# Kernel optimization log

Measured on AMD Instinct MI355X. Metric: run time of the kernel, lower is better.

## Reference

```python
import jax, jax.numpy as jnp
import numpy as np
from jax import lax

N, CIN, COUT, T, V, S = 64, 64, 64, 256, 25, 3
REL = CIN // 8  # 8, per __init__ branch for in_channels=64


def setup_inputs() -> dict:
    key = jax.random.key(0)
    ks = jax.random.split(key, 22)
    rn = lambda i, shape, s=0.05: jax.random.normal(ks[i], shape, jnp.float32) * s
    return dict(
        x=jax.random.normal(ks[0], (N, CIN, T, V), jnp.float32),
        A=rn(1, (S, V, V), 0.2),                 # adaptive PA parameter
        alpha=jnp.asarray(0.1, jnp.float32),     # unit_gcn alpha (scalar)
        w1=rn(2, (S, REL, CIN)), b1=rn(3, (S, REL)),
        w2=rn(4, (S, REL, CIN)), b2=rn(5, (S, REL)),
        w3=rn(6, (S, COUT, CIN)), b3=rn(7, (S, COUT)),
        w4=rn(8, (S, COUT, REL)), b4=rn(9, (S, COUT)),
        pm_w1=rn(10, (S, REL, 2 * REL)), pm_b1=rn(11, (S, REL)),
        pm_w2=rn(12, (S, REL, REL)), pm_b2=rn(13, (S, REL)),
        dw_w=rn(14, (S, REL, 1, 3, 3)),          # depthwise 3x3, groups=REL
        proj_w=rn(15, (S, COUT, REL)),           # aux_proj, no bias
        beta=rn(16, (S,), 0.01), gamma=rn(17, (S,), 0.01),
        bn_w=jnp.ones((COUT,), jnp.float32), bn_b=jnp.zeros((COUT,), jnp.float32),
    )


def _sorgc(x, Ai, alpha, w1, b1, w2, b2, w3, b3, w4, b4,
           pw1, pb1, pw2, pb2, dww, pjw, beta, gamma):
    # x: (N, C, T, V)
    xm = x.mean(axis=2)                                            # (N,C,V) -- 1x1 conv is linear, so conv then mean == mean then conv
    x1 = jnp.einsum('ncv,rc->nrv', xm, w1) + b1[:, None]           # (N,R,V)
    x2 = jnp.einsum('ncv,rc->nrv', xm, w2) + b2[:, None]
    x3 = jnp.einsum('nctv,oc->notv', x, w3) + b3[:, None, None]    # (N,O,T,V)
    q1 = jnp.tanh(x1[:, :, :, None] - x2[:, :, None, :])           # (N,R,V,V)
    psi = jnp.broadcast_to(x2[:, :, :, None], q1.shape)
    phi = jnp.broadcast_to(x2[:, :, None, :], q1.shape)
    pair = jnp.concatenate([psi, phi], axis=1)                     # (N,2R,V,V)
    h = jax.nn.relu(jnp.einsum('npuv,rp->nruv', pair, pw1) + pb1[:, None, None])
    q2 = jnp.einsum('npuv,rp->nruv', h, pw2) + pb2[:, None, None]
    q_all = q1 + gamma * q2
    R = (jnp.einsum('nruv,or->nouv', q_all, w4) + b4[:, None, None]) * alpha + Ai[None, None]
    # aux branch: depthwise 3x3 conv -> avgpool3x3 (count_include_pad) -> tanh -> 1x1 proj
    Ra = lax.conv_general_dilated(q1, dww, (1, 1), [(1, 1), (1, 1)],
                                  dimension_numbers=('NCHW', 'OIHW', 'NCHW'),
                                  feature_group_count=q1.shape[1])
    Ra = lax.reduce_window(Ra, 0.0, lax.add, (1, 1, 3, 3), (1, 1, 1, 1),
                           [(0, 0), (0, 0), (1, 1), (1, 1)]) / 9.0
    Ra = jnp.tanh(Ra)
    Ra = jnp.einsum('nruv,or->nouv', Ra, pjw)                      # (N,O,V,V)
    R = R + beta * Ra
    return jnp.einsum('ncuv,nctv->nctu', R, x3)                    # (N,O,T,V)


def reference(x, A, alpha, w1, b1, w2, b2, w3, b3, w4, b4,
              pm_w1, pm_b1, pm_w2, pm_b2, dw_w, proj_w, beta, gamma, bn_w, bn_b):
    y = None
    for i in range(S):
        z = _sorgc(x, A[i], alpha, w1[i], b1[i], w2[i], b2[i], w3[i], b3[i],
                   w4[i], b4[i], pm_w1[i], pm_b1[i], pm_w2[i], pm_b2[i],
                   dw_w[i], proj_w[i], beta[i], gamma[i])
        y = z if y is None else y + z
    # BatchNorm2d (training-mode batch statistics), eps=1e-5
    mu = y.mean(axis=(0, 2, 3), keepdims=True)
    var = y.var(axis=(0, 2, 3), keepdims=True)
    y = (y - mu) * lax.rsqrt(var + 1e-5) * bn_w[None, :, None, None] + bn_b[None, :, None, None]
    y = y + x  # residual (in_channels == out_channels -> identity down)
    return jax.nn.relu(y)
```

## Files before the change

kernel.cpp:

```cpp
#include <hip/hip_runtime.h>


#define WS_R_BYTE   409600
#define WS_BN_BYTE  17711104

typedef __attribute__((ext_vector_type(8))) short bf16x8;
typedef __attribute__((ext_vector_type(4))) float f32x4;

static __device__ __forceinline__ unsigned short f2bf(float f) {
    unsigned int u = __float_as_uint(f);
    u += 0x7fff + ((u >> 16) & 1);
    return (unsigned short)(u >> 16);
}
static __device__ __forceinline__ float bf2f(unsigned short s) {
    return __uint_as_float(((unsigned int)s) << 16);
}

__global__ __launch_bounds__(256) void k_xm(const float* __restrict__ x,
                                            float* __restrict__ ws) {
    int idx = blockIdx.x * 256 + threadIdx.x;
    int n = idx / 1600;
    int cv = idx % 1600;
    int c = cv / 25, v = cv % 25;
    const float* xp = x + (n * 64 + c) * 6400 + v;
    float s = 0.f;
    #pragma unroll 8
    for (int t = 0; t < 256; t++) s += xp[t * 25];
    ws[idx] = s * (1.f / 256.f);
}

__global__ __launch_bounds__(512) void k_small(
    const float* __restrict__ ws, unsigned short* __restrict__ Rg,
    const float* __restrict__ A, const float* __restrict__ alphap,
    const float* __restrict__ w1, const float* __restrict__ b1,
    const float* __restrict__ w2, const float* __restrict__ b2,
    const float* __restrict__ w4, const float* __restrict__ b4,
    const float* __restrict__ pw1, const float* __restrict__ pb1,
    const float* __restrict__ pw2, const float* __restrict__ pb2,
    const float* __restrict__ dww, const float* __restrict__ pjw,
    const float* __restrict__ beta, const float* __restrict__ gamma) {
    __shared__ float sm[15000];
    const int tid = threadIdx.x;
    const int s = blockIdx.x >> 6;
    const int n = blockIdx.x & 63;
    const float alpha = alphap[0];
    const float gam = gamma[s], bet = beta[s];

    for (int i = tid; i < 1600; i += 512) sm[5000 + i] = ws[n * 1600 + i];
    __syncthreads();

    for (int i = tid; i < 400; i += 512) {
        int half = i / 200, j = i % 200;
        int r = j / 25, k = j % 25;
        const float* w = (half ? w2 : w1) + (s * 8 + r) * 64;
        float acc = (half ? b2 : b1)[s * 8 + r];
        for (int c = 0; c < 64; c++) acc += w[c] * sm[5000 + c * 25 + k];
        sm[6600 + i] = acc;
    }
    __syncthreads();

    for (int i = tid; i < 5400; i += 512) {
        if (i < 5000) {
            int r = i / 625, uv = i % 625, u = uv / 25, v = uv % 25;
            sm[i] = tanhf(sm[6600 + r * 25 + u] - sm[6800 + r * 25 + v]);
        } else {
            int i2 = i - 5000;
            int half = i2 / 200, j = i2 % 200;
            int r = j / 25, k = j % 25;
            float acc = 0.f;
            for (int p = 0; p < 8; p++)
                acc += pw1[(s * 8 + r) * 16 + half * 8 + p] * sm[6800 + p * 25 + k];
            sm[7000 + i2] = acc;
        }
    }
    __syncthreads();

    for (int i = tid; i < 5000; i += 512) {
        int r = i / 625, uv = i % 625, u = uv / 25, v = uv % 25;
        float t = sm[7000 + r * 25 + u] + sm[7200 + r * 25 + v] + pb1[s * 8 + r];
        sm[10000 + i] = t > 0.f ? t : 0.f;
    }
    __syncthreads();

    for (int i = tid; i < 5000; i += 512) {
        int r = i / 625, uv = i % 625;
        float q2 = pb2[s * 8 + r];
        for (int p = 0; p < 8; p++)
            q2 += pw2[(s * 8 + r) * 8 + p] * sm[10000 + p * 625 + uv];
        sm[5000 + i] = sm[i] + gam * q2;
    }
    __syncthreads();

    for (int i = tid; i < 5000; i += 512) {
        int r = i / 625, uv = i % 625, u = uv / 25, v = uv % 25;
        float acc = 0.f;
        for (int di = 0; di < 3; di++) {
            int uu = u + di - 1;
            if (uu < 0 || uu > 24) continue;
            for (int dj = 0; dj < 3; dj++) {
                int vv = v + dj - 1;
                if (vv < 0 || vv > 24) continue;
                acc += sm[r * 625 + uu * 25 + vv] * dww[(s * 8 + r) * 9 + di * 3 + dj];
            }
        }
        sm[10000 + i] = acc;
    }
    __syncthreads();

    for (int i = tid; i < 5000; i += 512) {
        int r = i / 625, uv = i % 625, u = uv / 25, v = uv % 25;
        float acc = 0.f;
        for (int di = 0; di < 3; di++) {
            int uu = u + di - 1;
            if (uu < 0 || uu > 24) continue;
            for (int dj = 0; dj < 3; dj++) {
                int vv = v + dj - 1;
                if (vv < 0 || vv > 24) continue;
                acc += sm[10000 + r * 625 + uu * 25 + vv];
            }
        }
        sm[i] = tanhf(acc * (1.f / 9.f));
    }
    __syncthreads();

    unsigned short* Rb = Rg + (unsigned)((s * 64 + n) * 64) * 704;
    for (int i = tid; i < 40000; i += 512) {
        int o = i / 625, vu = i % 625, vv = vu / 25, uu = vu % 25;
        int quv = uu * 25 + vv;
        float mn = b4[s * 64 + o], aux = 0.f;
        for (int r = 0; r < 8; r++) {
            mn  += w4[(s * 64 + o) * 8 + r] * sm[5000 + r * 625 + quv];
            aux += pjw[(s * 64 + o) * 8 + r] * sm[r * 625 + quv];
        }
        Rb[o * 704 + vv * 28 + uu] = f2bf(mn * alpha + A[s * 625 + quv] + bet * aux);
    }
    for (int i = tid; i < 64 * 25 * 3; i += 512) {
        int o = i / 75, rem = i % 75, vv = rem / 3, uu = 25 + rem % 3;
        Rb[o * 704 + vv * 28 + uu] = 0;
    }
}

__global__ __launch_bounds__(256, 2) void k_main(
    const float* __restrict__ x, const float* __restrict__ w3,
    const float* __restrict__ b3, const unsigned short* __restrict__ Rg,
    float* __restrict__ out) {
    __shared__ __align__(16) unsigned short xb[400 * 64];
    __shared__ __align__(16) unsigned short Rs[64 * 84];
    const int tid  = threadIdx.x;
    const int n    = blockIdx.x >> 4;
    const int t0   = (blockIdx.x & 15) * 16;
    const int lane = tid & 63;
    const int w    = tid >> 6;
    const int ln15 = lane & 15;
    const int q    = lane >> 4;
    const int og   = w * 16 + ln15;

    {
        const float* xbase = x + n * 409600 + t0 * 25;
        #pragma unroll 5
        for (int k = 0; k < 25; k++) {
            int i  = tid + k * 256;
            int tv = i % 400;
            int cq = i / 400;
            const float* p = xbase + cq * 4 * 6400 + tv;
            ushort4 h;
            h.x = f2bf(p[0]); h.y = f2bf(p[6400]); h.z = f2bf(p[12800]); h.w = f2bf(p[19200]);
            int addr = tv * 64 + (((cq >> 1) ^ (tv & 7)) << 3) + ((cq & 1) << 2);
            *(ushort4*)&xb[addr] = h;
        }
    }

    float yacc[26][4];
    #pragma unroll
    for (int u = 0; u < 26; u++)
        #pragma unroll
        for (int r = 0; r < 4; r++) yacc[u][r] = 0.f;

    for (int s = 0; s < 3; s++) {
        bf16x8 bfr[2];
        {
            const float* wp = w3 + (s * 64 + og) * 64;
            #pragma unroll
            for (int ks = 0; ks < 2; ks++)
                #pragma unroll
                for (int j = 0; j < 8; j++)
                    bfr[ks][j] = (short)f2bf(wp[ks * 32 + q * 8 + j]);
        }
        const float bias = b3[s * 64 + og];
        const unsigned short* Rsrc = Rg + (unsigned)((s * 64 + n) * 64) * 704;

        for (int vg = 0; vg < 9; vg++) {
            const int nv = (vg < 8) ? 3 : 1;
            __syncthreads();
            {
                const int cpo = 7 * nv;
                const int nchunks = 64 * cpo;
                for (int i = tid; i < nchunks; i += 256) {
                    int o = i / cpo, ch = i % cpo;
                    *(ushort4*)&Rs[o * 84 + ch * 4] =
                        *(const ushort4*)&Rsrc[o * 704 + vg * 84 + ch * 4];
                }
            }
            __syncthreads();

            f32x4 c[3];
            #pragma unroll
            for (int iv = 0; iv < 3; iv++) {
                if (iv >= nv) break;
                const int v   = vg * 3 + iv;
                const int row = ln15 * 25 + v;
                const int sw  = row & 7;
                bf16x8 a0 = *(const bf16x8*)&xb[row * 64 + ((q ^ sw) << 3)];
                bf16x8 a1 = *(const bf16x8*)&xb[row * 64 + (((4 + q) ^ sw) << 3)];
                f32x4 cc; cc[0] = bias; cc[1] = bias; cc[2] = bias; cc[3] = bias;
                cc = __builtin_amdgcn_mfma_f32_16x16x32_bf16(a0, bfr[0], cc, 0, 0, 0);
                cc = __builtin_amdgcn_mfma_f32_16x16x32_bf16(a1, bfr[1], cc, 0, 0, 0);
                c[iv] = cc;
            }
            #pragma unroll
            for (int iv = 0; iv < 3; iv++) {
                if (iv >= nv) break;
                const unsigned short* rr = &Rs[og * 84 + iv * 28];
                f32x4 cc = c[iv];
                #pragma unroll
                for (int ug = 0; ug < 6; ug++) {
                    ushort4 r4 = *(const ushort4*)(rr + ug * 4);
                    float f0 = bf2f(r4.x), f1 = bf2f(r4.y);
                    float f2 = bf2f(r4.z), f3 = bf2f(r4.w);
                    #pragma unroll
                    for (int r = 0; r < 4; r++) {
                        yacc[ug * 4 + 0][r] += f0 * cc[r];
                        yacc[ug * 4 + 1][r] += f1 * cc[r];
                        yacc[ug * 4 + 2][r] += f2 * cc[r];
                        yacc[ug * 4 + 3][r] += f3 * cc[r];
                    }
                }
                float f24 = bf2f(rr[24]);
                #pragma unroll
                for (int r = 0; r < 4; r++) yacc[24][r] += f24 * cc[r];
            }
        }
    }

    float* op = out + (n * 64 + og) * 6400 + t0 * 25;
    #pragma unroll
    for (int r = 0; r < 4; r++) {
        float* opr = op + (q * 4 + r) * 25;
        #pragma unroll
        for (int u = 0; u < 25; u++) opr[u] = yacc[u][r];
    }
}

__global__ __launch_bounds__(256) void k_bnstat(const float* __restrict__ y,
                                                float* __restrict__ bnacc) {
    const int tid = threadIdx.x;
    const int o = blockIdx.x >> 3;
    const int ch = blockIdx.x & 7;
    float s = 0.f, s2 = 0.f;
    for (int nn = 0; nn < 8; nn++) {
        const int n = ch * 8 + nn;
        const float4* p = (const float4*)(y + (n * 64 + o) * 6400);
        for (int i = tid; i < 1600; i += 256) {
            float4 v = p[i];
            s  += v.x + v.y + v.z + v.w;
            s2 += v.x * v.x + v.y * v.y + v.z * v.z + v.w * v.w;
        }
    }
    for (int off = 32; off > 0; off >>= 1) {
        s  += __shfl_down(s, off);
        s2 += __shfl_down(s2, off);
    }
    __shared__ float ls[4], ls2[4];
    int wid = tid >> 6;
    if ((tid & 63) == 0) { ls[wid] = s; ls2[wid] = s2; }
    __syncthreads();
    if (tid == 0) {
        atomicAdd(bnacc + o,      ls[0] + ls[1] + ls[2] + ls[3]);
        atomicAdd(bnacc + 64 + o, ls2[0] + ls2[1] + ls2[2] + ls2[3]);
    }
}

__global__ __launch_bounds__(256) void k_final(
    float* __restrict__ out, const float* __restrict__ x,
    const float* __restrict__ bnacc,
    const float* __restrict__ bnw, const float* __restrict__ bnb) {
    const int idx4 = blockIdx.x * 256 + threadIdx.x;
    const int o = (idx4 / 1600) & 63;
    const float cnt = 1.f / 409600.f;
    float mean = bnacc[o] * cnt;
    float var = bnacc[64 + o] * cnt - mean * mean;
    float inv = rsqrtf(var + 1e-5f);
    float sc = bnw[o] * inv;
    float sh = bnb[o] - mean * sc;
    float4 y = ((const float4*)out)[idx4];
    float4 xv = ((const float4*)x)[idx4];
    y.x = fmaxf(y.x * sc + sh + xv.x, 0.f);
    y.y = fmaxf(y.y * sc + sh + xv.y, 0.f);
    y.z = fmaxf(y.z * sc + sh + xv.z, 0.f);
    y.w = fmaxf(y.w * sc + sh + xv.w, 0.f);
    ((float4*)out)[idx4] = y;
}

extern "C" void kernel_launch(void* const* d_in, const int* in_sizes, int n_in,
                              void* d_out, int out_size, void* d_ws, size_t ws_size,
                              hipStream_t stream) {
    const float* x     = (const float*)d_in[0];
    const float* A     = (const float*)d_in[1];
    const float* alpha = (const float*)d_in[2];
    const float* w1    = (const float*)d_in[3];
    const float* b1    = (const float*)d_in[4];
    const float* w2    = (const float*)d_in[5];
    const float* b2    = (const float*)d_in[6];
    const float* w3    = (const float*)d_in[7];
    const float* b3    = (const float*)d_in[8];
    const float* w4    = (const float*)d_in[9];
    const float* b4    = (const float*)d_in[10];
    const float* pw1   = (const float*)d_in[11];
    const float* pb1   = (const float*)d_in[12];
    const float* pw2   = (const float*)d_in[13];
    const float* pb2   = (const float*)d_in[14];
    const float* dww   = (const float*)d_in[15];
    const float* pjw   = (const float*)d_in[16];
    const float* beta  = (const float*)d_in[17];
    const float* gamma = (const float*)d_in[18];
    const float* bnw   = (const float*)d_in[19];
    const float* bnb   = (const float*)d_in[20];
    float* out = (float*)d_out;
    float* ws  = (float*)d_ws;
    unsigned short* wsR = (unsigned short*)((char*)d_ws + WS_R_BYTE);
    float* wsBN = (float*)((char*)d_ws + WS_BN_BYTE);

    k_xm<<<400, 256, 0, stream>>>(x, ws);
    k_small<<<192, 512, 0, stream>>>(ws, wsR, A, alpha, w1, b1, w2, b2,
                                     w4, b4, pw1, pb1, pw2, pb2, dww, pjw,
                                     beta, gamma);
    hipMemsetAsync(wsBN, 0, 128 * sizeof(float), stream);
    k_main<<<1024, 256, 0, stream>>>(x, w3, b3, wsR, out);
    k_bnstat<<<512, 256, 0, stream>>>(out, wsBN);
    k_final<<<25600, 256, 0, stream>>>(out, x, wsBN, bnw, bnb);
}
```

Baseline: 533.7 us.

## Fuse BN statistics into main kernel, read R directly from global, raise occupancy

```diff
diff --git a/kernel.cpp b/kernel.cpp
--- a/kernel.cpp
+++ b/kernel.cpp
@@ -2,10 +2,10 @@
 
 
 #define WS_R_BYTE   409600
-#define WS_BN_BYTE  17711104
 
 typedef __attribute__((ext_vector_type(8))) short bf16x8;
 typedef __attribute__((ext_vector_type(4))) float f32x4;
+typedef __attribute__((ext_vector_type(2))) float f32x2;
 
 static __device__ __forceinline__ unsigned short f2bf(float f) {
     unsigned int u = __float_as_uint(f);
@@ -140,12 +140,11 @@
     }
 }
 
-__global__ __launch_bounds__(256, 2) void k_main(
+__global__ __launch_bounds__(256, 3) void k_main(
     const float* __restrict__ x, const float* __restrict__ w3,
     const float* __restrict__ b3, const unsigned short* __restrict__ Rg,
-    float* __restrict__ out) {
+    float* __restrict__ out, float* __restrict__ bnacc) {
     __shared__ __align__(16) unsigned short xb[400 * 64];
-    __shared__ __align__(16) unsigned short Rs[64 * 84];
     const int tid  = threadIdx.x;
     const int n    = blockIdx.x >> 4;
     const int t0   = (blockIdx.x & 15) * 16;
@@ -169,12 +168,14 @@
             *(ushort4*)&xb[addr] = h;
         }
     }
-
-    float yacc[26][4];
+    __syncthreads();
+
+    f32x2 yacc[25][2];
     #pragma unroll
-    for (int u = 0; u < 26; u++)
-        #pragma unroll
-        for (int r = 0; r < 4; r++) yacc[u][r] = 0.f;
+    for (int u = 0; u < 25; u++) {
+        yacc[u][0] = (f32x2){0.f, 0.f};
+        yacc[u][1] = (f32x2){0.f, 0.f};
+    }
 
     for (int s = 0; s < 3; s++) {
         bf16x8 bfr[2];
@@ -187,96 +188,68 @@
                     bfr[ks][j] = (short)f2bf(wp[ks * 32 + q * 8 + j]);
         }
         const float bias = b3[s * 64 + og];
-        const unsigned short* Rsrc = Rg + (unsigned)((s * 64 + n) * 64) * 704;
-
-        for (int vg = 0; vg < 9; vg++) {
-            const int nv = (vg < 8) ? 3 : 1;
-            __syncthreads();
-            {
-                const int cpo = 7 * nv;
-                const int nchunks = 64 * cpo;
-                for (int i = tid; i < nchunks; i += 256) {
-                    int o = i / cpo, ch = i % cpo;
-                    *(ushort4*)&Rs[o * 84 + ch * 4] =
-                        *(const ushort4*)&Rsrc[o * 704 + vg * 84 + ch * 4];
-                }
+        const unsigned short* rrbase =
+            Rg + ((unsigned)((s * 64 + n) * 64 + og)) * 704;
+
+        for (int v = 0; v < 25; v++) {
+            const int row = ln15 * 25 + v;
+            const int sw  = row & 7;
+            bf16x8 a0 = *(const bf16x8*)&xb[row * 64 + ((q ^ sw) << 3)];
+            bf16x8 a1 = *(const bf16x8*)&xb[row * 64 + (((4 + q) ^ sw) << 3)];
+            f32x4 cc; cc[0] = bias; cc[1] = bias; cc[2] = bias; cc[3] = bias;
+            cc = __builtin_amdgcn_mfma_f32_16x16x32_bf16(a0, bfr[0], cc, 0, 0, 0);
+            cc = __builtin_amdgcn_mfma_f32_16x16x32_bf16(a1, bfr[1], cc, 0, 0, 0);
+            f32x2 c0; c0[0] = cc[0]; c0[1] = cc[1];
+            f32x2 c1; c1[0] = cc[2]; c1[1] = cc[3];
+
+            const unsigned short* rr = rrbase + v * 28;
+            #pragma unroll
+            for (int ug = 0; ug < 6; ug++) {
+                ushort4 r4 = *(const ushort4*)(rr + ug * 4);
+                float f0 = bf2f(r4.x), f1 = bf2f(r4.y);
+                float f2 = bf2f(r4.z), f3 = bf2f(r4.w);
+                yacc[ug * 4 + 0][0] += f0 * c0; yacc[ug * 4 + 0][1] += f0 * c1;
+                yacc[ug * 4 + 1][0] += f1 * c0; yacc[ug * 4 + 1][1] += f1 * c1;
+                yacc[ug * 4 + 2][0] += f2 * c0; yacc[ug * 4 + 2][1] += f2 * c1;
+                yacc[ug * 4 + 3][0] += f3 * c0; yacc[ug * 4 + 3][1] += f3 * c1;
             }
-            __syncthreads();
-
-            f32x4 c[3];
-            #pragma unroll
-            for (int iv = 0; iv < 3; iv++) {
-                if (iv >= nv) break;
-                const int v   = vg * 3 + iv;
-                const int row = ln15 * 25 + v;
-                const int sw  = row & 7;
-                bf16x8 a0 = *(const bf16x8*)&xb[row * 64 + ((q ^ sw) << 3)];
-                bf16x8 a1 = *(const bf16x8*)&xb[row * 64 + (((4 + q) ^ sw) << 3)];
-                f32x4 cc; cc[0] = bias; cc[1] = bias; cc[2] = bias; cc[3] = bias;
-                cc = __builtin_amdgcn_mfma_f32_16x16x32_bf16(a0, bfr[0], cc, 0, 0, 0);
-                cc = __builtin_amdgcn_mfma_f32_16x16x32_bf16(a1, bfr[1], cc, 0, 0, 0);
-                c[iv] = cc;
-            }
-            #pragma unroll
-            for (int iv = 0; iv < 3; iv++) {
-                if (iv >= nv) break;
-                const unsigned short* rr = &Rs[og * 84 + iv * 28];
-                f32x4 cc = c[iv];
-                #pragma unroll
-                for (int ug = 0; ug < 6; ug++) {
-                    ushort4 r4 = *(const ushort4*)(rr + ug * 4);
-                    float f0 = bf2f(r4.x), f1 = bf2f(r4.y);
-                    float f2 = bf2f(r4.z), f3 = bf2f(r4.w);
-                    #pragma unroll
-                    for (int r = 0; r < 4; r++) {
-                        yacc[ug * 4 + 0][r] += f0 * cc[r];
-                        yacc[ug * 4 + 1][r] += f1 * cc[r];
-                        yacc[ug * 4 + 2][r] += f2 * cc[r];
-                        yacc[ug * 4 + 3][r] += f3 * cc[r];
-                    }
-                }
-                float f24 = bf2f(rr[24]);
-                #pragma unroll
-                for (int r = 0; r < 4; r++) yacc[24][r] += f24 * cc[r];
-            }
+            float f24 = bf2f(rr[24]);
+            yacc[24][0] += f24 * c0;
+            yacc[24][1] += f24 * c1;
         }
     }
 
     float* op = out + (n * 64 + og) * 6400 + t0 * 25;
     #pragma unroll
-    for (int r = 0; r < 4; r++) {
-        float* opr = op + (q * 4 + r) * 25;
+    for (int h = 0; h < 2; h++) {
         #pragma unroll
-        for (int u = 0; u < 25; u++) opr[u] = yacc[u][r];
-    }
-}
-
-__global__ __launch_bounds__(256) void k_bnstat(const float* __restrict__ y,
-                                                float* __restrict__ bnacc) {
-    const int tid = threadIdx.x;
-    const int o = blockIdx.x >> 3;
-    const int ch = blockIdx.x & 7;
-    float s = 0.f, s2 = 0.f;
-    for (int nn = 0; nn < 8; nn++) {
-        const int n = ch * 8 + nn;
-        const float4* p = (const float4*)(y + (n * 64 + o) * 6400);
-        for (int i = tid; i < 1600; i += 256) {
-            float4 v = p[i];
-            s  += v.x + v.y + v.z + v.w;
-            s2 += v.x * v.x + v.y * v.y + v.z * v.z + v.w * v.w;
-        }
-    }
-    for (int off = 32; off > 0; off >>= 1) {
-        s  += __shfl_down(s, off);
-        s2 += __shfl_down(s2, off);
-    }
-    __shared__ float ls[4], ls2[4];
-    int wid = tid >> 6;
-    if ((tid & 63) == 0) { ls[wid] = s; ls2[wid] = s2; }
-    __syncthreads();
-    if (tid == 0) {
-        atomicAdd(bnacc + o,      ls[0] + ls[1] + ls[2] + ls[3]);
-        atomicAdd(bnacc + 64 + o, ls2[0] + ls2[1] + ls2[2] + ls2[3]);
+        for (int c = 0; c < 2; c++) {
+            float* opr = op + (q * 4 + h * 2 + c) * 25;
+            #pragma unroll
+            for (int ug = 0; ug < 6; ug++) {
+                float st[4] = {yacc[ug * 4 + 0][h][c], yacc[ug * 4 + 1][h][c],
+                               yacc[ug * 4 + 2][h][c], yacc[ug * 4 + 3][h][c]};
+                __builtin_memcpy(opr + ug * 4, st, 16);
+            }
+            opr[24] = yacc[24][h][c];
+        }
+    }
+
+    float s1 = 0.f, s2 = 0.f;
+    #pragma unroll
+    for (int u = 0; u < 25; u++) {
+        #pragma unroll
+        for (int h = 0; h < 2; h++) {
+            f32x2 yv = yacc[u][h];
+            s1 += yv[0] + yv[1];
+            s2 += yv[0] * yv[0] + yv[1] * yv[1];
+        }
+    }
+    s1 += __shfl_xor(s1, 16); s1 += __shfl_xor(s1, 32);
+    s2 += __shfl_xor(s2, 16); s2 += __shfl_xor(s2, 32);
+    if (q == 0) {
+        atomicAdd(&bnacc[og * 16], s1);
+        atomicAdd(&bnacc[1024 + og * 16], s2);
     }
 }
 
@@ -287,8 +260,8 @@
     const int idx4 = blockIdx.x * 256 + threadIdx.x;
     const int o = (idx4 / 1600) & 63;
     const float cnt = 1.f / 409600.f;
-    float mean = bnacc[o] * cnt;
-    float var = bnacc[64 + o] * cnt - mean * mean;
+    float mean = bnacc[o * 16] * cnt;
+    float var = bnacc[1024 + o * 16] * cnt - mean * mean;
     float inv = rsqrtf(var + 1e-5f);
     float sc = bnw[o] * inv;
     float sh = bnb[o] - mean * sc;
@@ -328,14 +301,13 @@
     float* out = (float*)d_out;
     float* ws  = (float*)d_ws;
     unsigned short* wsR = (unsigned short*)((char*)d_ws + WS_R_BYTE);
-    float* wsBN = (float*)((char*)d_ws + WS_BN_BYTE);
+    float* wsBN = ws;
 
     k_xm<<<400, 256, 0, stream>>>(x, ws);
     k_small<<<192, 512, 0, stream>>>(ws, wsR, A, alpha, w1, b1, w2, b2,
                                      w4, b4, pw1, pb1, pw2, pb2, dww, pjw,
                                      beta, gamma);
-    hipMemsetAsync(wsBN, 0, 128 * sizeof(float), stream);
-    k_main<<<1024, 256, 0, stream>>>(x, w3, b3, wsR, out);
-    k_bnstat<<<512, 256, 0, stream>>>(out, wsBN);
+    hipMemsetAsync(wsBN, 0, 8192, stream);
+    k_main<<<1024, 256, 0, stream>>>(x, w3, b3, wsR, out, wsBN);
     k_final<<<25600, 256, 0, stream>>>(out, x, wsBN, bnw, bnb);
 }
```

Measured after the change: 523.4 us. Within noise of the previous version (-1.9%).
